# Performance work log

Measured on AMD Instinct MI355X. Metric: run time of the kernel, lower is better.

## Reference

```python
import jax, jax.numpy as jnp
import numpy as np

NUM_HEADS = 16

def _rms_norm(x):
    # F.rms_norm over last dim, eps = dtype machine epsilon (torch default eps=None)
    eps = jnp.finfo(jnp.float32).eps
    ms = jnp.mean(jnp.square(x.astype(jnp.float32)), axis=-1, keepdims=True)
    return (x.astype(jnp.float32) * jax.lax.rsqrt(ms + eps)).astype(x.dtype)

def _rotary_tables(T, head_dim):
    # inv_freq = (1/1024)**linspace(0,1,head_dim//4), padded with zeros to head_dim//2
    quarter = head_dim // 4
    inv_freq = (1.0 / 1024.0) ** jnp.linspace(0.0, 1.0, quarter, dtype=jnp.float32)
    inv_freq = jnp.concatenate([inv_freq, jnp.zeros(quarter, dtype=jnp.float32)])
    t = jnp.arange(T, dtype=jnp.float32)
    theta = t[:, None] * inv_freq[None, :]          # [T, head_dim//2]
    return jnp.cos(theta), jnp.sin(theta)

def _rotary(x, cos, sin):
    # x: [B, T, H, hd]; rotate in fp32, cast back
    xf = x.astype(jnp.float32)
    x1, x2 = jnp.split(xf, 2, axis=-1)
    c = cos[None, :, None, :]
    s = sin[None, :, None, :]
    y1 = x1 * c + x2 * s
    y2 = -x1 * s + x2 * c
    return jnp.concatenate([y1, y2], axis=-1).astype(x.dtype)

def setup_inputs() -> dict:
    key = jax.random.key(0)
    ks = jax.random.split(key, 7)
    B, T, D = 1, 2048, 1024
    sc = 1.0 / np.sqrt(D)
    return {
        "x": jax.random.normal(ks[0], (B, T, D), jnp.float32),
        "vi": jax.random.normal(ks[1], (B, T, D), jnp.float32),
        "Wq": jax.random.normal(ks[2], (D, D), jnp.float32) * sc,
        "Wk": jax.random.normal(ks[3], (D, D), jnp.float32) * sc,
        "Wv": jax.random.normal(ks[4], (D, D), jnp.float32) * sc,
        "Wproj": jax.random.normal(ks[5], (D, D), jnp.float32) * sc,
        "lambdas": jnp.array([0.5, 0.5], jnp.float32),
    }

def reference(x, vi, Wq, Wk, Wv, Wproj, lambdas):
    B, T, D = x.shape
    H = NUM_HEADS
    hd = D // H
    q = (x @ Wq.T).reshape(B, T, H, hd)
    k = (x @ Wk.T).reshape(B, T, H, hd)
    v = (x @ Wv.T).reshape(B, T, H, hd)
    # value residual: lambda-mixed v
    v = lambdas[0] * v + lambdas[1] * vi.reshape(B, T, H, hd)
    q, k = _rms_norm(q), _rms_norm(k)
    cos, sin = _rotary_tables(T, hd)
    q, k = _rotary(q, cos, sin), _rotary(k, cos, sin)
    # causal attention, default flex_attention scale = 1/sqrt(head_dim)
    scores = jnp.einsum('bthd,bshd->bhts', q, k) / jnp.sqrt(jnp.float32(hd))
    causal = jnp.tril(jnp.ones((T, T), dtype=bool))
    scores = jnp.where(causal[None, None], scores, jnp.float32(-1e30))
    attn = jax.nn.softmax(scores, axis=-1)
    y = jnp.einsum('bhts,bshd->bthd', attn, v).reshape(B, T, D)
    return y @ Wproj.T
```

## Files before the change

kernel.cpp:

```cpp
#include <hip/hip_runtime.h>
#include <math.h>

#define T_SEQ 2048
#define D_MODEL 1024
#define NH 16
#define HD 64

typedef unsigned short ushort_t;
typedef unsigned int uint_t;
typedef short short8 __attribute__((ext_vector_type(8)));
typedef float floatx4 __attribute__((ext_vector_type(4)));

__device__ __forceinline__ ushort_t f2bf(float f) {
    uint_t u = __float_as_uint(f);
    u += 0x7FFFu + ((u >> 16) & 1u);
    return (ushort_t)(u >> 16);
}
__device__ __forceinline__ uint_t pack2(float a, float b) {
    return (uint_t)f2bf(a) | ((uint_t)f2bf(b) << 16);
}
__device__ __forceinline__ void cp16(ushort_t* dst, const ushort_t* src) {
    uint4 a = ((const uint4*)src)[0];
    uint4 b = ((const uint4*)src)[1];
    ((uint4*)dst)[0] = a;
    ((uint4*)dst)[1] = b;
}
__device__ __forceinline__ void gload16(const ushort_t* g, ushort_t* l) {
    __builtin_amdgcn_global_load_lds(
        (const __attribute__((address_space(1))) void*)g,
        (__attribute__((address_space(3))) void*)l, 16, 0, 0);
}

#define LDK 72

__global__ __launch_bounds__(256) void to_bf16(
        const float* __restrict__ x,  const float* __restrict__ wq,
        const float* __restrict__ wk, const float* __restrict__ wv,
        const float* __restrict__ wp,
        ushort_t* __restrict__ xb,  ushort_t* __restrict__ wqb,
        ushort_t* __restrict__ wkb, ushort_t* __restrict__ wvb,
        ushort_t* __restrict__ wpb)
{
    size_t i = (size_t)blockIdx.x * 256 + threadIdx.x;
    const float* src; ushort_t* dst; size_t off;
    if (i < 262144)      { src = x;  dst = xb;  off = i; }
    else if (i < 393216) { src = wq; dst = wqb; off = i - 262144; }
    else if (i < 524288) { src = wk; dst = wkb; off = i - 393216; }
    else if (i < 655360) { src = wv; dst = wvb; off = i - 524288; }
    else                 { src = wp; dst = wpb; off = i - 655360; }
    float4 f0 = ((const float4*)src)[off * 2];
    float4 f1 = ((const float4*)src)[off * 2 + 1];
    uint4 u;
    u.x = pack2(f0.x, f0.y); u.y = pack2(f0.z, f0.w);
    u.z = pack2(f1.x, f1.y); u.w = pack2(f1.z, f1.w);
    ((uint4*)dst)[off] = u;
}

__global__ __launch_bounds__(256) void gemm_qkv(
        const ushort_t* __restrict__ xb,
        const ushort_t* __restrict__ Wqb, const ushort_t* __restrict__ Wkb,
        const ushort_t* __restrict__ Wvb,
        const float* __restrict__ vi, const float* __restrict__ lam,
        ushort_t* __restrict__ qb, ushort_t* __restrict__ kb,
        ushort_t* __restrict__ vbt)
{
    const int z = blockIdx.z;
    const ushort_t* __restrict__ W = (z == 0) ? Wqb : (z == 1) ? Wkb : Wvb;
    const int row0 = blockIdx.y * 64;
    const int col0 = blockIdx.x * 128;

    __shared__ ushort_t As[64 * 64];
    __shared__ ushort_t Bs[128 * 64];

    const int tid = threadIdx.x;
    const int wave = tid >> 6, lane = tid & 63;
    const int wm = wave >> 1, wn = wave & 1;
    const int l15 = lane & 15, quad = lane >> 4;
    const int srow  = tid >> 3;
    const int sslot = (tid & 7) ^ (srow & 7);

    floatx4 acc[2][4];
    #pragma unroll
    for (int i = 0; i < 2; ++i)
        #pragma unroll
        for (int j = 0; j < 4; ++j)
            acc[i][j] = (floatx4){0.f, 0.f, 0.f, 0.f};

    for (int k0 = 0; k0 < D_MODEL; k0 += 64) {
        __syncthreads();
        #pragma unroll
        for (int c = 0; c < 2; ++c)
            gload16(xb + (size_t)(row0 + c * 32 + srow) * D_MODEL + k0 + sslot * 8,
                    As + c * 2048 + tid * 8);
        #pragma unroll
        for (int c = 0; c < 4; ++c)
            gload16(W + (size_t)(col0 + c * 32 + srow) * D_MODEL + k0 + sslot * 8,
                    Bs + c * 2048 + tid * 8);
        __syncthreads();
        #pragma unroll
        for (int kh = 0; kh < 2; ++kh) {
            const int slot = ((kh * 4 + quad) ^ (l15 & 7)) << 3;
            short8 a[2], b[4];
            #pragma unroll
            for (int i = 0; i < 2; ++i)
                a[i] = *(const short8*)(As + (32 * wm + i * 16 + l15) * 64 + slot);
            #pragma unroll
            for (int j = 0; j < 4; ++j)
                b[j] = *(const short8*)(Bs + (64 * wn + j * 16 + l15) * 64 + slot);
            #pragma unroll
            for (int i = 0; i < 2; ++i)
                #pragma unroll
                for (int j = 0; j < 4; ++j)
                    acc[i][j] = __builtin_amdgcn_mfma_f32_16x16x32_bf16(a[i], b[j], acc[i][j], 0, 0, 0);
        }
    }

    if (z < 2) {
        ushort_t* __restrict__ o = (z == 0) ? qb : kb;
        const float oscale = (z == 0) ? 0.125f : 1.0f;
        const int hbase = col0 + 64 * wn;
        const float eps = 1.1920929e-7f;
        const float fr = exp2f(-10.0f * (float)l15 / 15.0f);
        #pragma unroll
        for (int i = 0; i < 2; ++i)
            #pragma unroll
            for (int r = 0; r < 4; ++r) {
                const int t = row0 + 32 * wm + i * 16 + quad * 4 + r;
                float v0 = acc[i][0][r], v1 = acc[i][1][r];
                float v2 = acc[i][2][r], v3 = acc[i][3][r];
                float ss = v0 * v0 + v1 * v1 + v2 * v2 + v3 * v3;
                ss += __shfl_xor(ss, 1);
                ss += __shfl_xor(ss, 2);
                ss += __shfl_xor(ss, 4);
                ss += __shfl_xor(ss, 8);
                const float sc = rsqrtf(ss * (1.0f / 64.0f) + eps);
                v0 *= sc; v1 *= sc; v2 *= sc; v3 *= sc;
                const float th = (float)t * fr;
                const float cs = cosf(th), sn = sinf(th);
                const float y0 = v0 * cs + v2 * sn;
                const float y2 = v2 * cs - v0 * sn;
                const size_t rb = (size_t)t * D_MODEL + hbase;
                o[rb +  0 + l15] = f2bf(y0 * oscale);
                o[rb + 16 + l15] = f2bf(v1 * oscale);
                o[rb + 32 + l15] = f2bf(y2 * oscale);
                o[rb + 48 + l15] = f2bf(v3 * oscale);
            }
    } else {
        const float l0 = lam[0], l1 = lam[1];
        #pragma unroll
        for (int i = 0; i < 2; ++i)
            #pragma unroll
            for (int j = 0; j < 4; ++j) {
                const int tb = row0 + 32 * wm + i * 16 + quad * 4;
                const int jj = col0 + 64 * wn + j * 16 + l15;
                float b0 = l0 * acc[i][j][0] + l1 * vi[(size_t)(tb + 0) * D_MODEL + jj];
                float b1 = l0 * acc[i][j][1] + l1 * vi[(size_t)(tb + 1) * D_MODEL + jj];
                float b2 = l0 * acc[i][j][2] + l1 * vi[(size_t)(tb + 2) * D_MODEL + jj];
                float b3 = l0 * acc[i][j][3] + l1 * vi[(size_t)(tb + 3) * D_MODEL + jj];
                uint2 u;
                u.x = pack2(b0, b1);
                u.y = pack2(b2, b3);
                *(uint2*)(vbt + (size_t)jj * T_SEQ + tb) = u;
            }
    }
}

__global__ __launch_bounds__(256) void attn(
        const ushort_t* __restrict__ qb, const ushort_t* __restrict__ kb,
        const ushort_t* __restrict__ vbt, ushort_t* __restrict__ yb,
        float* __restrict__ Opart, float* __restrict__ Lpart)
{
    const int h = blockIdx.y;
    const int x = blockIdx.x;
    int qt, ct_begin, ct_end, pidx;
    if (x < 16) {
        qt = 31 - x;
        const int mid = (qt + 2) >> 1;
        ct_begin = 0; ct_end = mid;
        pidx = ((h * 16 + (qt - 16)) << 1);
    } else if (x < 32) {
        qt = 47 - x;
        const int mid = (qt + 2) >> 1;
        ct_begin = mid; ct_end = qt + 1;
        pidx = ((h * 16 + (qt - 16)) << 1) + 1;
    } else {
        qt = 47 - x;
        ct_begin = 0; ct_end = qt + 1;
        pidx = -1;
    }
    const int t0 = qt * 64;

    __shared__ ushort_t Ks[64 * LDK];
    __shared__ ushort_t Vs[64 * LDK];
    __shared__ ushort_t QPs[64 * LDK];

    const int tid = threadIdx.x;
    const int wave = tid >> 6, lane = tid & 63;
    const int l15 = lane & 15, quad = lane >> 4;
    const int r4 = tid >> 2, c4 = (tid & 3) * 16;

    cp16(QPs + r4 * LDK + c4, qb + (size_t)(t0 + r4) * D_MODEL + h * HD + c4);
    __syncthreads();
    short8 qf[2];
    qf[0] = *(const short8*)(QPs + (16 * wave + l15) * LDK + 0  + quad * 8);
    qf[1] = *(const short8*)(QPs + (16 * wave + l15) * LDK + 32 + quad * 8);

    float l_acc[4];
    floatx4 O[4];
    #pragma unroll
    for (int r = 0; r < 4; ++r) l_acc[r] = 0.0f;
    #pragma unroll
    for (int d = 0; d < 4; ++d) O[d] = (floatx4){0.f, 0.f, 0.f, 0.f};

    for (int kt = ct_begin; kt < ct_end; ++kt) {
        const int s0 = kt * 64;
        __syncthreads();
        cp16(Ks + r4 * LDK + c4, kb  + (size_t)(s0 + r4) * D_MODEL + h * HD + c4);
        cp16(Vs + r4 * LDK + c4, vbt + (size_t)(h * HD + r4) * T_SEQ + s0 + c4);
        __syncthreads();

        floatx4 sa[4];
        #pragma unroll
        for (int ct = 0; ct < 4; ++ct) {
            short8 b0 = *(const short8*)(Ks + (ct * 16 + l15) * LDK + 0  + quad * 8);
            short8 b1 = *(const short8*)(Ks + (ct * 16 + l15) * LDK + 32 + quad * 8);
            floatx4 t4 = (floatx4){0.f, 0.f, 0.f, 0.f};
            t4 = __builtin_amdgcn_mfma_f32_16x16x32_bf16(qf[0], b0, t4, 0, 0, 0);
            t4 = __builtin_amdgcn_mfma_f32_16x16x32_bf16(qf[1], b1, t4, 0, 0, 0);
            sa[ct] = t4;
        }
        if (kt == qt) {
            #pragma unroll
            for (int ct = 0; ct < 4; ++ct)
                #pragma unroll
                for (int r = 0; r < 4; ++r) {
                    int trow = 16 * wave + quad * 4 + r;
                    int scol = ct * 16 + l15;
                    if (scol > trow) sa[ct][r] = -1e30f;
                }
        }
        float p[4][4];
        #pragma unroll
        for (int ct = 0; ct < 4; ++ct)
            #pragma unroll
            for (int r = 0; r < 4; ++r) {
                p[ct][r] = __expf(sa[ct][r] - 8.0f);
                l_acc[r] += p[ct][r];
            }

        #pragma unroll
        for (int ct = 0; ct < 4; ++ct)
            #pragma unroll
            for (int r = 0; r < 4; ++r)
                QPs[(16 * wave + quad * 4 + r) * LDK + ct * 16 + l15] = f2bf(p[ct][r]);

        short8 pa0 = *(const short8*)(QPs + (16 * wave + l15) * LDK + 0  + quad * 8);
        short8 pa1 = *(const short8*)(QPs + (16 * wave + l15) * LDK + 32 + quad * 8);
        #pragma unroll
        for (int dt = 0; dt < 4; ++dt) {
            short8 vb0 = *(const short8*)(Vs + (dt * 16 + l15) * LDK + 0  + quad * 8);
            short8 vb1 = *(const short8*)(Vs + (dt * 16 + l15) * LDK + 32 + quad * 8);
            O[dt] = __builtin_amdgcn_mfma_f32_16x16x32_bf16(pa0, vb0, O[dt], 0, 0, 0);
            O[dt] = __builtin_amdgcn_mfma_f32_16x16x32_bf16(pa1, vb1, O[dt], 0, 0, 0);
        }
    }

    float l_run[4];
    #pragma unroll
    for (int r = 0; r < 4; ++r) {
        float s = l_acc[r];
        s += __shfl_xor(s, 1);
        s += __shfl_xor(s, 2);
        s += __shfl_xor(s, 4);
        s += __shfl_xor(s, 8);
        l_run[r] = s;
    }

    if (pidx < 0) {
        #pragma unroll
        for (int r = 0; r < 4; ++r) {
            const float inv_l = 1.0f / l_run[r];
            const int t = t0 + 16 * wave + quad * 4 + r;
            #pragma unroll
            for (int dt = 0; dt < 4; ++dt)
                yb[(size_t)t * D_MODEL + h * HD + dt * 16 + l15] = f2bf(O[dt][r] * inv_l);
        }
    } else {
        float* __restrict__ Op = Opart + (size_t)pidx * 4096;
        #pragma unroll
        for (int r = 0; r < 4; ++r) {
            const int row = 16 * wave + quad * 4 + r;
            #pragma unroll
            for (int dt = 0; dt < 4; ++dt)
                Op[row * 64 + dt * 16 + l15] = O[dt][r];
            if (l15 == 0) Lpart[(size_t)pidx * 64 + row] = l_run[r];
        }
    }
}

__global__ __launch_bounds__(256) void attn_combine(
        const float* __restrict__ Opart, const float* __restrict__ Lpart,
        ushort_t* __restrict__ yb)
{
    const int qtp = blockIdx.x;
    const int h   = blockIdx.y;
    const int tid = threadIdx.x;
    const int row  = tid >> 2;
    const int dseg = (tid & 3) * 16;
    const int p0 = (h * 16 + qtp) * 2;

    const float l0 = Lpart[(size_t)p0 * 64 + row];
    const float l1 = Lpart[((size_t)p0 + 1) * 64 + row];
    const float inv = 1.0f / (l0 + l1);

    const float* O0 = Opart + (size_t)p0 * 4096 + row * 64 + dseg;
    const float* O1 = O0 + 4096;

    uint_t u[8];
    #pragma unroll
    for (int g = 0; g < 4; ++g) {
        float4 a = ((const float4*)O0)[g];
        float4 b = ((const float4*)O1)[g];
        u[g * 2 + 0] = pack2((a.x + b.x) * inv, (a.y + b.y) * inv);
        u[g * 2 + 1] = pack2((a.z + b.z) * inv, (a.w + b.w) * inv);
    }
    const int t = (16 + qtp) * 64 + row;
    uint4* dst = (uint4*)(yb + (size_t)t * D_MODEL + h * HD + dseg);
    dst[0] = make_uint4(u[0], u[1], u[2], u[3]);
    dst[1] = make_uint4(u[4], u[5], u[6], u[7]);
}

__global__ __launch_bounds__(256) void gemm_proj(
        const ushort_t* __restrict__ yb, const ushort_t* __restrict__ Wpb,
        float* __restrict__ out)
{
    const int row0 = blockIdx.y * 64;
    const int col0 = blockIdx.x * 128;

    __shared__ ushort_t As[64 * 64];
    __shared__ ushort_t Bs[128 * 64];

    const int tid = threadIdx.x;
    const int wave = tid >> 6, lane = tid & 63;
    const int wm = wave >> 1, wn = wave & 1;
    const int l15 = lane & 15, quad = lane >> 4;
    const int srow  = tid >> 3;
    const int sslot = (tid & 7) ^ (srow & 7);

    floatx4 acc[2][4];
    #pragma unroll
    for (int i = 0; i < 2; ++i)
        #pragma unroll
        for (int j = 0; j < 4; ++j)
            acc[i][j] = (floatx4){0.f, 0.f, 0.f, 0.f};

    for (int k0 = 0; k0 < D_MODEL; k0 += 64) {
        __syncthreads();
        #pragma unroll
        for (int c = 0; c < 2; ++c)
            gload16(yb + (size_t)(row0 + c * 32 + srow) * D_MODEL + k0 + sslot * 8,
                    As + c * 2048 + tid * 8);
        #pragma unroll
        for (int c = 0; c < 4; ++c)
            gload16(Wpb + (size_t)(col0 + c * 32 + srow) * D_MODEL + k0 + sslot * 8,
                    Bs + c * 2048 + tid * 8);
        __syncthreads();
        #pragma unroll
        for (int kh = 0; kh < 2; ++kh) {
            const int slot = ((kh * 4 + quad) ^ (l15 & 7)) << 3;
            short8 a[2], b[4];
            #pragma unroll
            for (int i = 0; i < 2; ++i)
                a[i] = *(const short8*)(As + (32 * wm + i * 16 + l15) * 64 + slot);
            #pragma unroll
            for (int j = 0; j < 4; ++j)
                b[j] = *(const short8*)(Bs + (64 * wn + j * 16 + l15) * 64 + slot);
            #pragma unroll
            for (int i = 0; i < 2; ++i)
                #pragma unroll
                for (int j = 0; j < 4; ++j)
                    acc[i][j] = __builtin_amdgcn_mfma_f32_16x16x32_bf16(a[i], b[j], acc[i][j], 0, 0, 0);
        }
    }

    #pragma unroll
    for (int i = 0; i < 2; ++i)
        #pragma unroll
        for (int j = 0; j < 4; ++j) {
            const int t = row0 + 32 * wm + i * 16 + quad * 4;
            const int jj = col0 + 64 * wn + j * 16 + l15;
            #pragma unroll
            for (int r = 0; r < 4; ++r)
                out[(size_t)(t + r) * D_MODEL + jj] = acc[i][j][r];
        }
}

extern "C" void kernel_launch(void* const* d_in, const int* in_sizes, int n_in,
                              void* d_out, int out_size, void* d_ws, size_t ws_size,
                              hipStream_t stream) {
    (void)in_sizes; (void)n_in; (void)out_size; (void)ws_size;
    const float* x   = (const float*)d_in[0];
    const float* vi  = (const float*)d_in[1];
    const float* Wq  = (const float*)d_in[2];
    const float* Wk  = (const float*)d_in[3];
    const float* Wv  = (const float*)d_in[4];
    const float* Wp  = (const float*)d_in[5];
    const float* lam = (const float*)d_in[6];

    char* base = (char*)d_ws;
    ushort_t* xb  = (ushort_t*)(base);
    ushort_t* wqb = (ushort_t*)(base + (size_t)4  * 1048576);
    ushort_t* wkb = (ushort_t*)(base + (size_t)6  * 1048576);
    ushort_t* wvb = (ushort_t*)(base + (size_t)8  * 1048576);
    ushort_t* wpb = (ushort_t*)(base + (size_t)10 * 1048576);
    ushort_t* qb  = (ushort_t*)(base + (size_t)12 * 1048576);
    ushort_t* kb  = (ushort_t*)(base + (size_t)16 * 1048576);
    ushort_t* vbt = (ushort_t*)(base + (size_t)20 * 1048576);
    ushort_t* yb  = (ushort_t*)(base + (size_t)24 * 1048576);
    float* Opart  = (float*)(base);
    float* Lpart  = (float*)(base + (size_t)8 * 1048576);
    float* out = (float*)d_out;

    to_bf16<<<dim3(786432 / 256), 256, 0, stream>>>(x, Wq, Wk, Wv, Wp, xb, wqb, wkb, wvb, wpb);
    gemm_qkv<<<dim3(8, 32, 3), 256, 0, stream>>>(xb, wqb, wkb, wvb, vi, lam, qb, kb, vbt);
    attn<<<dim3(48, 16), 256, 0, stream>>>(qb, kb, vbt, yb, Opart, Lpart);
    attn_combine<<<dim3(16, 16), 256, 0, stream>>>(Opart, Lpart, yb);
    gemm_proj<<<dim3(8, 32), 256, 0, stream>>>(yb, wpb, out);
}
```

Baseline: 157.5 us.

## Double-buffer LDS tiles with async global loads in GEMMs and attention

Converts the QKV GEMM, projection GEMM and attention K/V loops to double-buffered shared memory. The next tile's global loads are issued before computing on the current tile, with explicit vmcnt waits and raw barriers, so load latency overlaps MFMA work. Attention K/V staging also switches from padded-row copies to an XOR-swizzled layout to avoid bank conflicts. This doubles LDS use per block, which may lower occupancy, and relies on gload16 being an async direct-to-LDS load so the vmcnt counts stay correct.

```diff
diff --git a/kernel.cpp b/kernel.cpp
--- a/kernel.cpp
+++ b/kernel.cpp
@@ -69,8 +69,8 @@
     const int row0 = blockIdx.y * 64;
     const int col0 = blockIdx.x * 128;
 
-    __shared__ ushort_t As[64 * 64];
-    __shared__ ushort_t Bs[128 * 64];
+    __shared__ ushort_t As[2 * 64 * 64];
+    __shared__ ushort_t Bs[2 * 128 * 64];
 
     const int tid = threadIdx.x;
     const int wave = tid >> 6, lane = tid & 63;
@@ -86,33 +86,51 @@
         for (int j = 0; j < 4; ++j)
             acc[i][j] = (floatx4){0.f, 0.f, 0.f, 0.f};
 
-    for (int k0 = 0; k0 < D_MODEL; k0 += 64) {
-        __syncthreads();
+    auto stageAB = [&](int k0, int p) {
+        ushort_t* Ap = As + p * 4096;
+        ushort_t* Bp = Bs + p * 8192;
         #pragma unroll
         for (int c = 0; c < 2; ++c)
             gload16(xb + (size_t)(row0 + c * 32 + srow) * D_MODEL + k0 + sslot * 8,
-                    As + c * 2048 + tid * 8);
+                    Ap + c * 2048 + tid * 8);
         #pragma unroll
         for (int c = 0; c < 4; ++c)
             gload16(W + (size_t)(col0 + c * 32 + srow) * D_MODEL + k0 + sslot * 8,
-                    Bs + c * 2048 + tid * 8);
-        __syncthreads();
+                    Bp + c * 2048 + tid * 8);
+    };
+
+    stageAB(0, 0);
+    int cur = 0;
+    for (int knext = 64; knext <= D_MODEL; knext += 64) {
+        const bool haveNext = (knext < D_MODEL);
+        if (haveNext) {
+            stageAB(knext, cur ^ 1);
+            asm volatile("s_waitcnt vmcnt(6)" ::: "memory");
+        } else {
+            asm volatile("s_waitcnt vmcnt(0)" ::: "memory");
+        }
+        __builtin_amdgcn_s_barrier();
+        const ushort_t* Ac = As + cur * 4096;
+        const ushort_t* Bc = Bs + cur * 8192;
         #pragma unroll
         for (int kh = 0; kh < 2; ++kh) {
             const int slot = ((kh * 4 + quad) ^ (l15 & 7)) << 3;
             short8 a[2], b[4];
             #pragma unroll
             for (int i = 0; i < 2; ++i)
-                a[i] = *(const short8*)(As + (32 * wm + i * 16 + l15) * 64 + slot);
+                a[i] = *(const short8*)(Ac + (32 * wm + i * 16 + l15) * 64 + slot);
             #pragma unroll
             for (int j = 0; j < 4; ++j)
-                b[j] = *(const short8*)(Bs + (64 * wn + j * 16 + l15) * 64 + slot);
+                b[j] = *(const short8*)(Bc + (64 * wn + j * 16 + l15) * 64 + slot);
             #pragma unroll
             for (int i = 0; i < 2; ++i)
                 #pragma unroll
                 for (int j = 0; j < 4; ++j)
                     acc[i][j] = __builtin_amdgcn_mfma_f32_16x16x32_bf16(a[i], b[j], acc[i][j], 0, 0, 0);
         }
+        asm volatile("" ::: "memory");
+        __builtin_amdgcn_s_barrier();
+        cur ^= 1;
     }
 
     if (z < 2) {
@@ -190,14 +208,17 @@
     }
     const int t0 = qt * 64;
 
-    __shared__ ushort_t Ks[64 * LDK];
-    __shared__ ushort_t Vs[64 * LDK];
+    __shared__ ushort_t Ks[2 * 64 * 64];
+    __shared__ ushort_t Vs[2 * 64 * 64];
     __shared__ ushort_t QPs[64 * LDK];
 
     const int tid = threadIdx.x;
     const int wave = tid >> 6, lane = tid & 63;
     const int l15 = lane & 15, quad = lane >> 4;
     const int r4 = tid >> 2, c4 = (tid & 3) * 16;
+    const int srow  = tid >> 3;
+    const int sslot = (tid & 7) ^ (srow & 7);
+    const int bx = l15 & 7;
 
     cp16(QPs + r4 * LDK + c4, qb + (size_t)(t0 + r4) * D_MODEL + h * HD + c4);
     __syncthreads();
@@ -205,6 +226,16 @@
     qf[0] = *(const short8*)(QPs + (16 * wave + l15) * LDK + 0  + quad * 8);
     qf[1] = *(const short8*)(QPs + (16 * wave + l15) * LDK + 32 + quad * 8);
 
+    auto stageKV = [&](int kt, int p) {
+        const int s0 = kt * 64;
+        ushort_t* Kp = Ks + p * 4096;
+        ushort_t* Vp = Vs + p * 4096;
+        gload16(kb  + (size_t)(s0 + srow)      * D_MODEL + h * HD + sslot * 8, Kp + tid * 8);
+        gload16(kb  + (size_t)(s0 + 32 + srow) * D_MODEL + h * HD + sslot * 8, Kp + 2048 + tid * 8);
+        gload16(vbt + (size_t)(h * HD + srow)      * T_SEQ + s0 + sslot * 8,   Vp + tid * 8);
+        gload16(vbt + (size_t)(h * HD + 32 + srow) * T_SEQ + s0 + sslot * 8,   Vp + 2048 + tid * 8);
+    };
+
     float l_acc[4];
     floatx4 O[4];
     #pragma unroll
@@ -212,18 +243,27 @@
     #pragma unroll
     for (int d = 0; d < 4; ++d) O[d] = (floatx4){0.f, 0.f, 0.f, 0.f};
 
+    stageKV(ct_begin, 0);
+    int cur = 0;
     for (int kt = ct_begin; kt < ct_end; ++kt) {
-        const int s0 = kt * 64;
-        __syncthreads();
-        cp16(Ks + r4 * LDK + c4, kb  + (size_t)(s0 + r4) * D_MODEL + h * HD + c4);
-        cp16(Vs + r4 * LDK + c4, vbt + (size_t)(h * HD + r4) * T_SEQ + s0 + c4);
-        __syncthreads();
+        const bool haveNext = (kt + 1 < ct_end);
+        if (haveNext) {
+            stageKV(kt + 1, cur ^ 1);
+            asm volatile("s_waitcnt vmcnt(4)" ::: "memory");
+        } else {
+            asm volatile("s_waitcnt vmcnt(0)" ::: "memory");
+        }
+        __builtin_amdgcn_s_barrier();
+
+        const ushort_t* Kc = Ks + cur * 4096;
+        const ushort_t* Vc = Vs + cur * 4096;
 
         floatx4 sa[4];
         #pragma unroll
         for (int ct = 0; ct < 4; ++ct) {
-            short8 b0 = *(const short8*)(Ks + (ct * 16 + l15) * LDK + 0  + quad * 8);
-            short8 b1 = *(const short8*)(Ks + (ct * 16 + l15) * LDK + 32 + quad * 8);
+            const ushort_t* krow = Kc + (ct * 16 + l15) * 64;
+            short8 b0 = *(const short8*)(krow + ((quad ^ bx) << 3));
+            short8 b1 = *(const short8*)(krow + (((quad + 4) ^ bx) << 3));
             floatx4 t4 = (floatx4){0.f, 0.f, 0.f, 0.f};
             t4 = __builtin_amdgcn_mfma_f32_16x16x32_bf16(qf[0], b0, t4, 0, 0, 0);
             t4 = __builtin_amdgcn_mfma_f32_16x16x32_bf16(qf[1], b1, t4, 0, 0, 0);
@@ -258,11 +298,16 @@
         short8 pa1 = *(const short8*)(QPs + (16 * wave + l15) * LDK + 32 + quad * 8);
         #pragma unroll
         for (int dt = 0; dt < 4; ++dt) {
-            short8 vb0 = *(const short8*)(Vs + (dt * 16 + l15) * LDK + 0  + quad * 8);
-            short8 vb1 = *(const short8*)(Vs + (dt * 16 + l15) * LDK + 32 + quad * 8);
+            const ushort_t* vrow = Vc + (dt * 16 + l15) * 64;
+            short8 vb0 = *(const short8*)(vrow + ((quad ^ bx) << 3));
+            short8 vb1 = *(const short8*)(vrow + (((quad + 4) ^ bx) << 3));
             O[dt] = __builtin_amdgcn_mfma_f32_16x16x32_bf16(pa0, vb0, O[dt], 0, 0, 0);
             O[dt] = __builtin_amdgcn_mfma_f32_16x16x32_bf16(pa1, vb1, O[dt], 0, 0, 0);
         }
+
+        asm volatile("" ::: "memory");
+        __builtin_amdgcn_s_barrier();
+        cur ^= 1;
     }
 
     float l_run[4];
@@ -337,8 +382,8 @@
     const int row0 = blockIdx.y * 64;
     const int col0 = blockIdx.x * 128;
 
-    __shared__ ushort_t As[64 * 64];
-    __shared__ ushort_t Bs[128 * 64];
+    __shared__ ushort_t As[2 * 64 * 64];
+    __shared__ ushort_t Bs[2 * 128 * 64];
 
     const int tid = threadIdx.x;
     const int wave = tid >> 6, lane = tid & 63;
@@ -354,33 +399,51 @@
         for (int j = 0; j < 4; ++j)
             acc[i][j] = (floatx4){0.f, 0.f, 0.f, 0.f};
 
-    for (int k0 = 0; k0 < D_MODEL; k0 += 64) {
-        __syncthreads();
+    auto stageAB = [&](int k0, int p) {
+        ushort_t* Ap = As + p * 4096;
+        ushort_t* Bp = Bs + p * 8192;
         #pragma unroll
         for (int c = 0; c < 2; ++c)
             gload16(yb + (size_t)(row0 + c * 32 + srow) * D_MODEL + k0 + sslot * 8,
-                    As + c * 2048 + tid * 8);
+                    Ap + c * 2048 + tid * 8);
         #pragma unroll
         for (int c = 0; c < 4; ++c)
             gload16(Wpb + (size_t)(col0 + c * 32 + srow) * D_MODEL + k0 + sslot * 8,
-                    Bs + c * 2048 + tid * 8);
-        __syncthreads();
+                    Bp + c * 2048 + tid * 8);
+    };
+
+    stageAB(0, 0);
+    int cur = 0;
+    for (int knext = 64; knext <= D_MODEL; knext += 64) {
+        const bool haveNext = (knext < D_MODEL);
+        if (haveNext) {
+            stageAB(knext, cur ^ 1);
+            asm volatile("s_waitcnt vmcnt(6)" ::: "memory");
+        } else {
+            asm volatile("s_waitcnt vmcnt(0)" ::: "memory");
+        }
+        __builtin_amdgcn_s_barrier();
+        const ushort_t* Ac = As + cur * 4096;
+        const ushort_t* Bc = Bs + cur * 8192;
         #pragma unroll
         for (int kh = 0; kh < 2; ++kh) {
             const int slot = ((kh * 4 + quad) ^ (l15 & 7)) << 3;
             short8 a[2], b[4];
             #pragma unroll
             for (int i = 0; i < 2; ++i)
-                a[i] = *(const short8*)(As + (32 * wm + i * 16 + l15) * 64 + slot);
+                a[i] = *(const short8*)(Ac + (32 * wm + i * 16 + l15) * 64 + slot);
             #pragma unroll
             for (int j = 0; j < 4; ++j)
-                b[j] = *(const short8*)(Bs + (64 * wn + j * 16 + l15) * 64 + slot);
+                b[j] = *(const short8*)(Bc + (64 * wn + j * 16 + l15) * 64 + slot);
             #pragma unroll
             for (int i = 0; i < 2; ++i)
                 #pragma unroll
                 for (int j = 0; j < 4; ++j)
                     acc[i][j] = __builtin_amdgcn_mfma_f32_16x16x32_bf16(a[i], b[j], acc[i][j], 0, 0, 0);
         }
+        asm volatile("" ::: "memory");
+        __builtin_amdgcn_s_barrier();
+        cur ^= 1;
     }
 
     #pragma unroll
```

Result: faster. 149.7 us (-5.0%).
